# Optimization experiments

Measured on AMD Instinct MI355X. Metric: run time of the kernel, lower is better.

## Reference

```python
import jax, jax.numpy as jnp
import numpy as np
from jax import lax

KSIZE = 3
STRIDE = 1
RATE = 2
FUSE_K = 3
SCALE = 10.0
DN = ('NCHW', 'OIHW', 'NCHW')


def _same_pad_amount(size, k, s):
    out = (size + s - 1) // s
    pad = max(0, (out - 1) * s + k - size)
    return pad // 2, pad - pad // 2


def extract_patches(x, k, s):
    # torch.nn.Unfold with 'same' padding; returns [B, L, C, k, k], L row-major
    B, C, H, W = x.shape
    pt, pb = _same_pad_amount(H, k, s)
    pl, pr = _same_pad_amount(W, k, s)
    xp = jnp.pad(x, ((0, 0), (0, 0), (pt, pb), (pl, pr)))
    Ho = (H + s - 1) // s
    Wo = (W + s - 1) // s
    rows = (jnp.arange(Ho) * s)[:, None] + jnp.arange(k)[None, :]  # [Ho,k]
    cols = (jnp.arange(Wo) * s)[:, None] + jnp.arange(k)[None, :]  # [Wo,k]
    p = xp[:, :, rows, :][:, :, :, :, cols]  # [B,C,Ho,k,Wo,k]
    return p.transpose(0, 2, 4, 1, 3, 5).reshape(B, Ho * Wo, C, k, k)


def setup_inputs() -> dict:
    key = jax.random.key(0)
    kf, kb = jax.random.split(key)
    f = jax.random.normal(kf, (2, 128, 128, 128), dtype=jnp.float32)
    b = jax.random.normal(kb, (2, 128, 128, 128), dtype=jnp.float32)
    mask = jnp.zeros((1, 1, 128, 128), dtype=jnp.float32)  # all patches available
    return {"f": f, "b": b, "mask": mask}


def reference(f, b, mask):
    B, C, Hr, Wr = f.shape
    kernel = 2 * RATE
    # raw background patches for final aggregation: [B, Lb, C, 4, 4]
    raw_w = extract_patches(b, kernel, RATE * STRIDE)
    # nearest downsample by rate (src_idx = i*rate)
    f_ds = f[:, :, ::RATE, ::RATE]
    b_ds = b[:, :, ::RATE, ::RATE]
    Hf, Wf = f_ds.shape[2], f_ds.shape[3]
    Hb, Wb = b_ds.shape[2], b_ds.shape[3]
    L = Hb * Wb
    # matching patches: [B, L, C, 3, 3]
    w = extract_patches(b_ds, KSIZE, STRIDE)
    # mask patches (shared across batch, torch uses m[0])
    m_ds = mask[:, :, ::RATE, ::RATE]
    m = extract_patches(m_ds, KSIZE, STRIDE)[0]  # [L,1,3,3]
    mm = (jnp.mean(m, axis=(1, 2, 3)) == 0.0).astype(f.dtype).reshape(1, L, 1, 1)
    # L2-normalize patch filters (escape_NaN added elementwise before sum, as in torch)
    wn = w / jnp.sqrt(jnp.sum(w * w + 1e-4, axis=(2, 3, 4), keepdims=True))

    def score_one(xi, wi):
        # xi [C,Hf,Wf], wi [L,C,3,3] -> [L,Hf,Wf]
        return lax.conv_general_dilated(xi[None], wi, (1, 1), [(1, 1), (1, 1)],
                                        dimension_numbers=DN)[0]

    y = jax.vmap(score_one)(f_ds, wn)  # [B, L, Hf, Wf]

    # diagonal fuse: identity 3x3 conv on the [L, Hf*Wf] score matrix, twice with transpose
    fw = jnp.eye(FUSE_K, dtype=f.dtype).reshape(1, 1, FUSE_K, FUSE_K)

    def fuse_conv(t):
        return lax.conv_general_dilated(t, fw, (1, 1), [(1, 1), (1, 1)],
                                        dimension_numbers=DN)

    y = y.reshape(B, 1, Hb * Wb, Hf * Wf)
    y = fuse_conv(y).reshape(B, Hb, Wb, Hf, Wf)
    y = y.transpose(0, 2, 1, 4, 3).reshape(B, 1, L, Hf * Wf)
    y = fuse_conv(y).reshape(B, Wb, Hb, Wf, Hf)
    y = y.transpose(0, 2, 1, 4, 3).reshape(B, L, Hf, Wf)

    y = y * mm
    y = jax.nn.softmax(y * SCALE, axis=1) * mm

    def deconv_one(a, wc):
        # conv_transpose2d(a, wc, stride=rate, padding=1); wc [L,C,4,4]
        wt = jnp.flip(wc, (-2, -1)).transpose(1, 0, 2, 3)  # [C,L,4,4]
        pad = kernel - 1 - 1
        return lax.conv_general_dilated(a[None], wt, (1, 1), [(pad, pad), (pad, pad)],
                                        lhs_dilation=(RATE, RATE),
                                        dimension_numbers=DN)[0]

    out = jax.vmap(deconv_one)(y, raw_w) / 4.0  # [B, C, Hr, Wr]
    return out
```

## Files before the change

### kernel.cpp

```cpp
#include <hip/hip_runtime.h>
#include <cstdint>

typedef _Float16 f16x8 __attribute__((ext_vector_type(8)));
typedef float f32x4 __attribute__((ext_vector_type(4)));

typedef __attribute__((address_space(1))) void gvoid;
typedef __attribute__((address_space(3))) void lvoid;

__device__ __forceinline__ void gload16(const void* g, void* l) {
    __builtin_amdgcn_global_load_lds((gvoid*)g, (lvoid*)l, 16, 0, 0);
}

__device__ __forceinline__ void bar() {
    asm volatile("" ::: "memory");
    __builtin_amdgcn_s_barrier();
    asm volatile("" ::: "memory");
}
#define WAITV(N) asm volatile("s_waitcnt vmcnt(" #N ")" ::: "memory")
#define WAITL(N) do { asm volatile("s_waitcnt lgkmcnt(" #N ")" ::: "memory"); \
                      __builtin_amdgcn_sched_barrier(0); } while (0)

__global__ __launch_bounds__(256) void downsample_kernel(const float* __restrict__ f,
                                                         const float* __restrict__ b,
                                                         float* __restrict__ fds,
                                                         float* __restrict__ bds) {
    int idx = blockIdx.x * 256 + threadIdx.x;
    const float* src = blockIdx.y ? b : f;
    float* dst = blockIdx.y ? bds : fds;
    int bb = idx >> 19;
    int r = idx & 524287;
    int c = r >> 12, a = (r >> 6) & 63, v = r & 63;
    dst[idx] = src[(size_t)bb * 2097152 + (size_t)c * 16384 + (2 * a) * 128 + 2 * v];
}

__global__ __launch_bounds__(256) void build_mm_kernel(const float* __restrict__ mask,
                                                       float* __restrict__ mm) {
    int l = blockIdx.x * 256 + threadIdx.x;
    if (l >= 4096) return;
    int i = l >> 6, j = l & 63;
    float s = 0.f;
    #pragma unroll
    for (int dy = 0; dy < 3; ++dy)
        #pragma unroll
        for (int dx = 0; dx < 3; ++dx) {
            int a = i + dy - 1, b = j + dx - 1;
            if ((unsigned)a < 64u && (unsigned)b < 64u)
                s += mask[(2 * a) * 128 + 2 * b];
        }
    mm[l] = (s == 0.0f) ? 1.0f : 0.0f;
}

__global__ __launch_bounds__(256) void build_fpatch_kernel(const float* __restrict__ fds,
                                                           _Float16* __restrict__ Fp) {
    int bb = blockIdx.x >> 12;
    int p = blockIdx.x & 4095;
    const float* fb = fds + (size_t)bb * 524288;
    _Float16* Fpb = Fp + (size_t)bb * 4718592;
    int u = p >> 6, v = p & 63;
    for (int k = threadIdx.x; k < 1152; k += 256) {
        int c = k / 9;
        int s = k - 9 * c;
        int dy = s / 3, dx = s - 3 * dy;
        int a = u + dy - 1, bcol = v + dx - 1;
        float val = 0.f;
        if ((unsigned)a < 64u && (unsigned)bcol < 64u)
            val = fb[c * 4096 + a * 64 + bcol];
        Fpb[(size_t)p * 1152 + k] = (_Float16)val;
    }
}

__global__ __launch_bounds__(256) void build_wn_kernel(const float* __restrict__ bds,
                                                       _Float16* __restrict__ Wn) {
    __shared__ float wsh[1152];
    __shared__ float red[4];
    int bb = blockIdx.x >> 12;
    int l = blockIdx.x & 4095;
    const float* bp = bds + (size_t)bb * 524288;
    _Float16* Wnb = Wn + (size_t)bb * 4718592;
    int i = l >> 6, j = l & 63;
    float sq = 0.f;
    for (int k = threadIdx.x; k < 1152; k += 256) {
        int c = k / 9;
        int s = k - 9 * c;
        int dy = s / 3, dx = s - 3 * dy;
        int a = i + dy - 1, bcol = j + dx - 1;
        float val = 0.f;
        if ((unsigned)a < 64u && (unsigned)bcol < 64u)
            val = bp[c * 4096 + a * 64 + bcol];
        wsh[k] = val;
        sq += val * val;
    }
    #pragma unroll
    for (int off = 32; off > 0; off >>= 1) sq += __shfl_xor(sq, off);
    if ((threadIdx.x & 63) == 0) red[threadIdx.x >> 6] = sq;
    __syncthreads();
    float total = red[0] + red[1] + red[2] + red[3] + 0.1152f;
    float rinv = 1.0f / sqrtf(total);
    for (int k = threadIdx.x; k < 1152; k += 256)
        Wnb[(size_t)l * 1152 + k] = (_Float16)(wsh[k] * rinv);
}

__global__ __launch_bounds__(256) void build_vt_kernel(const float* __restrict__ b,
                                                       _Float16* __restrict__ Vt) {
    int bb = blockIdx.x >> 11;
    int n = blockIdx.x & 2047;
    const float* bp = b + (size_t)bb * 2097152;
    _Float16* Vtb = Vt + (size_t)bb * 8388608;
    int c = n >> 4, r = n & 15, rh = r >> 2, rw = r & 3;
    const float* bc = bp + (size_t)c * 16384;
    for (int l = threadIdx.x; l < 4096; l += 256) {
        int lh = l >> 6, lw = l & 63;
        int row = 2 * lh + rh - 1, col = 2 * lw + rw - 1;
        float val = 0.f;
        if ((unsigned)row < 128u && (unsigned)col < 128u)
            val = bc[row * 128 + col];
        Vtb[(size_t)n * 4096 + l] = (_Float16)val;
    }
}

template <int KSTR, int NTILES>
__device__ __forceinline__ void gemm_core(const _Float16* __restrict__ A,
                                          const _Float16* __restrict__ Bt,
                                          _Float16* __restrict__ C,
                                          _Float16* __restrict__ AsB,
                                          _Float16* __restrict__ BsB) {
    const int tid = threadIdx.x;
    const int lane = tid & 63;
    const int wave = tid >> 6;
    const int quad = lane >> 4;
    const int l16 = lane & 15;
    const int wm = wave >> 2;
    const int wn = wave & 3;
    const int bm = blockIdx.y * 256;
    const int bn = blockIdx.x * 256;

    f32x4 acc[8][4] = {};
    f16x8 afrA[4], afrB[4], bfrA[4], bfrB[4];

    const int s0 = tid, s1 = 512 + tid;
    const int sr0 = s0 >> 2, sr1 = s1 >> 2;
    const int r0 = sr0 ^ ((sr0 >> 2) & 1);
    const int r1 = sr1 ^ ((sr1 >> 2) & 1);
    const int q0 = (s0 & 3) ^ (r0 & 3);
    const int q1 = (s1 & 3) ^ (r1 & 3);
    const int offA0 = (bm + r0) * KSTR + q0 * 8;
    const int offA1 = (bm + r1) * KSTR + q1 * 8;
    const int offB0 = (bn + r0) * KSTR + q0 * 8;
    const int offB1 = (bn + r1) * KSTR + q1 * 8;

#define STAGE_A(buf, kt, kh) do {                                                          \
        gload16(A + offA0 + (kt) * 64 + (kh) * 32, AsB + ((buf) * 2 + (kh)) * 8192 + tid * 8); \
        gload16(A + offA1 + (kt) * 64 + (kh) * 32, AsB + ((buf) * 2 + (kh)) * 8192 + 4096 + tid * 8); \
    } while (0)
#define STAGE_B(buf, kt, kh) do {                                                          \
        gload16(Bt + offB0 + (kt) * 64 + (kh) * 32, BsB + ((buf) * 2 + (kh)) * 8192 + tid * 8); \
        gload16(Bt + offB1 + (kt) * 64 + (kh) * 32, BsB + ((buf) * 2 + (kh)) * 8192 + 4096 + tid * 8); \
    } while (0)

    const int c2 = (l16 >> 2) & 1;
    const int rdoff = ((l16 ^ c2) * 32) + ((quad ^ (l16 & 3)) * 8);

#define LDA(dst, buf, kh, mh) do {                                                         \
        _Pragma("unroll")                                                                  \
        for (int mi = 0; mi < 4; ++mi)                                                     \
            dst[mi] = *(const f16x8*)&AsB[((buf) * 2 + (kh)) * 8192 +                      \
                (wm * 128 + ((mh) * 4 + mi) * 16) * 32 + rdoff];                           \
    } while (0)
#define LDB(dst, buf, kh) do {                                                             \
        _Pragma("unroll")                                                                  \
        for (int ni = 0; ni < 4; ++ni)                                                     \
            dst[ni] = *(const f16x8*)&BsB[((buf) * 2 + (kh)) * 8192 +                      \
                (wn * 64 + ni * 16) * 32 + rdoff];                                         \
    } while (0)
#define MM(af, bf, mh) do {                                                                \
        __builtin_amdgcn_s_setprio(1);                                                     \
        _Pragma("unroll")                                                                  \
        for (int mi = 0; mi < 4; ++mi)                                                     \
            _Pragma("unroll")                                                              \
            for (int ni = 0; ni < 4; ++ni)                                                 \
                acc[(mh) * 4 + mi][ni] = __builtin_amdgcn_mfma_f32_16x16x32_f16(           \
                    af[mi], bf[ni], acc[(mh) * 4 + mi][ni], 0, 0, 0);                      \
        __builtin_amdgcn_s_setprio(0);                                                     \
    } while (0)

    STAGE_A(0, 0, 0); STAGE_B(0, 0, 0);
    STAGE_A(0, 0, 1); STAGE_B(0, 0, 1);
    STAGE_A(1, 1, 0); STAGE_B(1, 1, 0);
    WAITV(4);
    bar();
    LDA(afrA, 0, 0, 0); LDB(bfrA, 0, 0);

    #pragma unroll 1
    for (int i = 0; i < NTILES / 2 - 1; ++i) {
        const int t0 = 2 * i;
        STAGE_A(1, t0 + 1, 1);
        bar();
        LDA(afrB, 0, 0, 1);
        WAITL(4);
        MM(afrA, bfrA, 0);
        bar();
        STAGE_B(1, t0 + 1, 1);
        bar();
        LDA(afrA, 0, 1, 0); LDB(bfrB, 0, 1);
        WAITL(8);
        MM(afrB, bfrA, 1);
        bar();
        STAGE_A(0, t0 + 2, 0);
        bar();
        LDA(afrB, 0, 1, 1);
        WAITL(4);
        MM(afrA, bfrB, 0);
        bar();
        STAGE_B(0, t0 + 2, 0); WAITV(4);
        bar();
        LDA(afrA, 1, 0, 0); LDB(bfrA, 1, 0);
        WAITL(8);
        MM(afrB, bfrB, 1);
        bar();
        STAGE_A(0, t0 + 2, 1);
        bar();
        LDA(afrB, 1, 0, 1);
        WAITL(4);
        MM(afrA, bfrA, 0);
        bar();
        STAGE_B(0, t0 + 2, 1);
        bar();
        LDA(afrA, 1, 1, 0); LDB(bfrB, 1, 1);
        WAITL(8);
        MM(afrB, bfrA, 1);
        bar();
        STAGE_A(1, t0 + 3, 0);
        bar();
        LDA(afrB, 1, 1, 1);
        WAITL(4);
        MM(afrA, bfrB, 0);
        bar();
        STAGE_B(1, t0 + 3, 0); WAITV(4);
        bar();
        LDA(afrA, 0, 0, 0); LDB(bfrA, 0, 0);
        WAITL(8);
        MM(afrB, bfrB, 1);
        bar();
    }

    STAGE_A(1, NTILES - 1, 1);
    bar();
    LDA(afrB, 0, 0, 1);
    WAITL(4);
    MM(afrA, bfrA, 0);
    bar();
    STAGE_B(1, NTILES - 1, 1);
    bar();
    LDA(afrA, 0, 1, 0); LDB(bfrB, 0, 1);
    WAITL(8);
    MM(afrB, bfrA, 1);
    bar();
    bar();
    LDA(afrB, 0, 1, 1);
    WAITL(4);
    MM(afrA, bfrB, 0);
    bar();
    WAITV(4);
    bar();
    LDA(afrA, 1, 0, 0); LDB(bfrA, 1, 0);
    WAITL(8);
    MM(afrB, bfrB, 1);
    bar();
    bar();
    LDA(afrB, 1, 0, 1);
    WAITL(4);
    MM(afrA, bfrA, 0);
    bar();
    WAITV(0);
    bar();
    LDA(afrA, 1, 1, 0); LDB(bfrB, 1, 1);
    WAITL(8);
    MM(afrB, bfrA, 1);
    bar();
    bar();
    LDA(afrB, 1, 1, 1);
    WAITL(4);
    MM(afrA, bfrB, 0);
    bar();
    WAITL(0);
    MM(afrB, bfrB, 1);

#undef STAGE_A
#undef STAGE_B
#undef LDA
#undef LDB
#undef MM

    #pragma unroll
    for (int mi = 0; mi < 8; ++mi)
        #pragma unroll
        for (int ni = 0; ni < 4; ++ni)
            #pragma unroll
            for (int r = 0; r < 4; ++r) {
                int row = bm + wm * 128 + mi * 16 + quad * 4 + r;
                int col = bn + wn * 64 + ni * 16 + l16;
                C[(size_t)row * 4096 + col] = (_Float16)acc[mi][ni][r];
            }
}

__global__ __launch_bounds__(512, 2) void gemm1_kernel(const _Float16* __restrict__ Fp,
                                                       const _Float16* __restrict__ Wn,
                                                       _Float16* __restrict__ S0) {
    __shared__ __align__(16) _Float16 As[2][2][8192];
    __shared__ __align__(16) _Float16 Bs[2][2][8192];
    const int z = blockIdx.z;
    gemm_core<1152, 18>(Fp + (size_t)z * 4718592, Wn + (size_t)z * 4718592,
                        S0 + (size_t)z * 16777216, &As[0][0][0], &Bs[0][0][0]);
}

__global__ __launch_bounds__(512, 2) void gemm2_kernel(const _Float16* __restrict__ Vt,
                                                       const _Float16* __restrict__ att0,
                                                       const _Float16* __restrict__ att1,
                                                       _Float16* __restrict__ OTh) {
    __shared__ __align__(16) _Float16 As[2][2][8192];
    __shared__ __align__(16) _Float16 Bs[2][2][8192];
    const int z = blockIdx.z;
    gemm_core<4096, 64>(Vt + (size_t)z * 8388608, z ? att1 : att0,
                        OTh + (size_t)z * 8388608, &As[0][0][0], &Bs[0][0][0]);
}

__global__ __launch_bounds__(256) void fuse_softmax_kernel(const _Float16* __restrict__ S0,
                                                           const float* __restrict__ mm,
                                                           _Float16* __restrict__ att0,
                                                           _Float16* __restrict__ att1) {
    __shared__ float red[4];
    const int tid = threadIdx.x;
    const int lane = tid & 63;
    const int wave = tid >> 6;
    int g = blockIdx.x;
    int p_global = ((g & 7) << 10) | (g >> 3);
    const int bb = p_global >> 12;
    const int p = p_global & 4095;
    const _Float16* S = S0 + (size_t)bb * 16777216;
    _Float16* att = bb ? att1 : att0;
    const int pbase = ((p & 63) << 6) | (p >> 6);

    float acc[16];
    #pragma unroll
    for (int k = 0; k < 16; ++k) acc[k] = 0.f;

    #pragma unroll
    for (int t2 = -1; t2 <= 1; ++t2) {
        int b2 = pbase + t2;
        if ((unsigned)b2 >= 4096u) continue;
        int pp = ((b2 & 63) << 6) | (b2 >> 6);
        #pragma unroll
        for (int t1 = -1; t1 <= 1; ++t1) {
            int rr = pp + t1;
            if ((unsigned)rr >= 4096u) continue;
            const _Float16* row = S + (size_t)rr * 4096;
            #pragma unroll
            for (int k = 0; k < 16; ++k) {
                int l = k * 256 + tid;
                int i = (k * 256 + wave * 64) >> 6;
                int it2 = i + t2;
                if (it2 >= 0 && it2 < 64) {
                    int c = l + t2 * 64 + t1;
                    if ((unsigned)c < 4096u)
                        acc[k] += (float)row[c];
                } else if (it2 == 64) {
                    if (lane <= 62) {
                        int c = lane + 1 + t1;
                        if ((unsigned)c < 4096u) acc[k] += (float)row[c];
                    }
                } else {
                    if (lane >= 1) {
                        int c = 4031 + lane + t1;
                        if ((unsigned)c < 4096u) acc[k] += (float)row[c];
                    }
                }
            }
        }
    }

    float mv[16];
    float lmax = -1e30f;
    #pragma unroll
    for (int k = 0; k < 16; ++k) {
        int l = k * 256 + tid;
        mv[k] = mm[l];
        float lg = acc[k] * mv[k] * 10.0f;
        acc[k] = lg;
        lmax = fmaxf(lmax, lg);
    }
    #pragma unroll
    for (int off = 32; off > 0; off >>= 1) lmax = fmaxf(lmax, __shfl_xor(lmax, off));
    if (lane == 0) red[wave] = lmax;
    __syncthreads();
    lmax = fmaxf(fmaxf(red[0], red[1]), fmaxf(red[2], red[3]));
    __syncthreads();

    float lsum = 0.f;
    #pragma unroll
    for (int k = 0; k < 16; ++k) {
        float e = __expf(acc[k] - lmax);
        acc[k] = e;
        lsum += e;
    }
    #pragma unroll
    for (int off = 32; off > 0; off >>= 1) lsum += __shfl_xor(lsum, off);
    if (lane == 0) red[wave] = lsum;
    __syncthreads();
    float inv = 1.0f / (red[0] + red[1] + red[2] + red[3]);
    #pragma unroll
    for (int k = 0; k < 16; ++k) {
        int l = k * 256 + tid;
        att[(size_t)p * 4096 + l] = (_Float16)(acc[k] * inv * mv[k]);
    }
}

__global__ __launch_bounds__(256) void assemble_kernel(const _Float16* __restrict__ OTh,
                                                       float* __restrict__ out) {
    int idx = blockIdx.x * 256 + threadIdx.x;
    int bb = idx >> 21;
    int w = idx & 2097151;
    const _Float16* OTb = OTh + (size_t)bb * 8388608;
    int x = w & 127, y = (w >> 7) & 127, c = w >> 14;
    int r0 = (y + 1) & 1, s0 = (x + 1) & 1;
    float acc = 0.f;
    #pragma unroll
    for (int a = 0; a < 2; ++a) {
        int rh = r0 + 2 * a;
        int ph = (y + 1 - rh) >> 1;
        if ((unsigned)ph < 64u) {
            #pragma unroll
            for (int bq = 0; bq < 2; ++bq) {
                int rw = s0 + 2 * bq;
                int pw = (x + 1 - rw) >> 1;
                if ((unsigned)pw < 64u)
                    acc += (float)OTb[(size_t)(c * 16 + rh * 4 + rw) * 4096 + ph * 64 + pw];
            }
        }
    }
    out[idx] = 0.25f * acc;
}

extern "C" void kernel_launch(void* const* d_in, const int* in_sizes, int n_in,
                              void* d_out, int out_size, void* d_ws, size_t ws_size,
                              hipStream_t stream) {
    const float* f = (const float*)d_in[0];
    const float* b = (const float*)d_in[1];
    const float* mask = (const float*)d_in[2];
    float* out = (float*)d_out;
    char* ws = (char*)d_ws;

    float* mm = (float*)ws;
    _Float16* Fp = (_Float16*)(ws + 16384);
    _Float16* Wn = (_Float16*)(ws + 16384 + 18874368);
    _Float16* att0 = (_Float16*)(ws + 16384);
    _Float16* S0 = (_Float16*)(ws + 37765120);
    _Float16* Vt = (_Float16*)(ws + 37765120);
    _Float16* OTh = (_Float16*)(ws + 37765120 + 33554432);
    float* fds = (float*)(ws + 104873984);
    float* bds = (float*)(ws + 104873984 + 4194304);
    _Float16* att1 = (_Float16*)(ws + 104873984);

    downsample_kernel<<<dim3(4096, 2), 256, 0, stream>>>(f, b, fds, bds);
    build_mm_kernel<<<16, 256, 0, stream>>>(mask, mm);
    build_fpatch_kernel<<<8192, 256, 0, stream>>>(fds, Fp);
    build_wn_kernel<<<8192, 256, 0, stream>>>(bds, Wn);

    gemm1_kernel<<<dim3(16, 16, 2), 512, 0, stream>>>(Fp, Wn, S0);
    fuse_softmax_kernel<<<8192, 256, 0, stream>>>(S0, mm, att0, att1);

    build_vt_kernel<<<4096, 256, 0, stream>>>(b, Vt);
    gemm2_kernel<<<dim3(16, 8, 2), 512, 0, stream>>>(Vt, att0, att1, OTh);
    assemble_kernel<<<16384, 256, 0, stream>>>(OTh, out);
}
```

Measured before the change: 440.3 us.

## Use 4-wave 128x128 warp tiles in GEMMs and vectorize fuse-softmax row access

The shared GEMM core drops from 8 waves to 4 waves per 256x256 block. Each wave now owns a 128x128 sub-tile with 8x8 accumulators, and each thread issues four async global-to-LDS loads per stage instead of two, with the wait counts adjusted to match. The fuse-softmax kernel changes so each thread handles 16 contiguous columns: it loads the neighbouring window with two 8-wide f16 vector loads and stores the results as vectors, replacing 16 strided scalar accesses. The aim is more MFMA work per LDS fragment load and fewer memory instructions. The cost is much higher register pressure and fewer waves to hide latency, with launch bounds set to 256 threads and 1 block.

New measurement: 470.7 us. 6.9% more time.

```diff
diff --git a/kernel.cpp b/kernel.cpp
--- a/kernel.cpp
+++ b/kernel.cpp
@@ -129,32 +129,36 @@
     const int wave = tid >> 6;
     const int quad = lane >> 4;
     const int l16 = lane & 15;
-    const int wm = wave >> 2;
-    const int wn = wave & 3;
+    const int wm = wave >> 1;
+    const int wn2 = wave & 1;
     const int bm = blockIdx.y * 256;
     const int bn = blockIdx.x * 256;
 
-    f32x4 acc[8][4] = {};
-    f16x8 afrA[4], afrB[4], bfrA[4], bfrB[4];
-
-    const int s0 = tid, s1 = 512 + tid;
-    const int sr0 = s0 >> 2, sr1 = s1 >> 2;
-    const int r0 = sr0 ^ ((sr0 >> 2) & 1);
-    const int r1 = sr1 ^ ((sr1 >> 2) & 1);
-    const int q0 = (s0 & 3) ^ (r0 & 3);
-    const int q1 = (s1 & 3) ^ (r1 & 3);
-    const int offA0 = (bm + r0) * KSTR + q0 * 8;
-    const int offA1 = (bm + r1) * KSTR + q1 * 8;
-    const int offB0 = (bn + r0) * KSTR + q0 * 8;
-    const int offB1 = (bn + r1) * KSTR + q1 * 8;
+    f32x4 acc[8][8] = {};
+    f16x8 afrA[4], afrB[4], bfrA[8], bfrB[8];
+
+    int offA[4], offB[4];
+    #pragma unroll
+    for (int rd = 0; rd < 4; ++rd) {
+        int s = rd * 256 + tid;
+        int sr = s >> 2;
+        int r = sr ^ ((sr >> 2) & 1);
+        int q = (s & 3) ^ (r & 3);
+        offA[rd] = (bm + r) * KSTR + q * 8;
+        offB[rd] = (bn + r) * KSTR + q * 8;
+    }
 
 #define STAGE_A(buf, kt, kh) do {                                                          \
-        gload16(A + offA0 + (kt) * 64 + (kh) * 32, AsB + ((buf) * 2 + (kh)) * 8192 + tid * 8); \
-        gload16(A + offA1 + (kt) * 64 + (kh) * 32, AsB + ((buf) * 2 + (kh)) * 8192 + 4096 + tid * 8); \
+        _Pragma("unroll")                                                                  \
+        for (int rd = 0; rd < 4; ++rd)                                                     \
+            gload16(A + offA[rd] + (kt) * 64 + (kh) * 32,                                  \
+                    AsB + ((buf) * 2 + (kh)) * 8192 + (rd * 256 + tid) * 8);               \
     } while (0)
 #define STAGE_B(buf, kt, kh) do {                                                          \
-        gload16(Bt + offB0 + (kt) * 64 + (kh) * 32, BsB + ((buf) * 2 + (kh)) * 8192 + tid * 8); \
-        gload16(Bt + offB1 + (kt) * 64 + (kh) * 32, BsB + ((buf) * 2 + (kh)) * 8192 + 4096 + tid * 8); \
+        _Pragma("unroll")                                                                  \
+        for (int rd = 0; rd < 4; ++rd)                                                     \
+            gload16(Bt + offB[rd] + (kt) * 64 + (kh) * 32,                                 \
+                    BsB + ((buf) * 2 + (kh)) * 8192 + (rd * 256 + tid) * 8);               \
     } while (0)
 
     const int c2 = (l16 >> 2) & 1;
@@ -168,16 +172,16 @@
     } while (0)
 #define LDB(dst, buf, kh) do {                                                             \
         _Pragma("unroll")                                                                  \
-        for (int ni = 0; ni < 4; ++ni)                                                     \
+        for (int ni = 0; ni < 8; ++ni)                                                     \
             dst[ni] = *(const f16x8*)&BsB[((buf) * 2 + (kh)) * 8192 +                      \
-                (wn * 64 + ni * 16) * 32 + rdoff];                                         \
+                (wn2 * 128 + ni * 16) * 32 + rdoff];                                       \
     } while (0)
 #define MM(af, bf, mh) do {                                                                \
         __builtin_amdgcn_s_setprio(1);                                                     \
         _Pragma("unroll")                                                                  \
         for (int mi = 0; mi < 4; ++mi)                                                     \
             _Pragma("unroll")                                                              \
-            for (int ni = 0; ni < 4; ++ni)                                                 \
+            for (int ni = 0; ni < 8; ++ni)                                                 \
                 acc[(mh) * 4 + mi][ni] = __builtin_amdgcn_mfma_f32_16x16x32_f16(           \
                     af[mi], bf[ni], acc[(mh) * 4 + mi][ni], 0, 0, 0);                      \
         __builtin_amdgcn_s_setprio(0);                                                     \
@@ -186,7 +190,7 @@
     STAGE_A(0, 0, 0); STAGE_B(0, 0, 0);
     STAGE_A(0, 0, 1); STAGE_B(0, 0, 1);
     STAGE_A(1, 1, 0); STAGE_B(1, 1, 0);
-    WAITV(4);
+    WAITV(8);
     bar();
     LDA(afrA, 0, 0, 0); LDB(bfrA, 0, 0);
 
@@ -202,7 +206,7 @@
         STAGE_B(1, t0 + 1, 1);
         bar();
         LDA(afrA, 0, 1, 0); LDB(bfrB, 0, 1);
-        WAITL(8);
+        WAITL(12);
         MM(afrB, bfrA, 1);
         bar();
         STAGE_A(0, t0 + 2, 0);
@@ -211,10 +215,10 @@
         WAITL(4);
         MM(afrA, bfrB, 0);
         bar();
-        STAGE_B(0, t0 + 2, 0); WAITV(4);
+        STAGE_B(0, t0 + 2, 0); WAITV(8);
         bar();
         LDA(afrA, 1, 0, 0); LDB(bfrA, 1, 0);
-        WAITL(8);
+        WAITL(12);
         MM(afrB, bfrB, 1);
         bar();
         STAGE_A(0, t0 + 2, 1);
@@ -226,7 +230,7 @@
         STAGE_B(0, t0 + 2, 1);
         bar();
         LDA(afrA, 1, 1, 0); LDB(bfrB, 1, 1);
-        WAITL(8);
+        WAITL(12);
         MM(afrB, bfrA, 1);
         bar();
         STAGE_A(1, t0 + 3, 0);
@@ -235,10 +239,10 @@
         WAITL(4);
         MM(afrA, bfrB, 0);
         bar();
-        STAGE_B(1, t0 + 3, 0); WAITV(4);
+        STAGE_B(1, t0 + 3, 0); WAITV(8);
         bar();
         LDA(afrA, 0, 0, 0); LDB(bfrA, 0, 0);
-        WAITL(8);
+        WAITL(12);
         MM(afrB, bfrB, 1);
         bar();
     }
@@ -252,7 +256,7 @@
     STAGE_B(1, NTILES - 1, 1);
     bar();
     LDA(afrA, 0, 1, 0); LDB(bfrB, 0, 1);
-    WAITL(8);
+    WAITL(12);
     MM(afrB, bfrA, 1);
     bar();
     bar();
@@ -260,10 +264,10 @@
     WAITL(4);
     MM(afrA, bfrB, 0);
     bar();
-    WAITV(4);
+    WAITV(8);
     bar();
     LDA(afrA, 1, 0, 0); LDB(bfrA, 1, 0);
-    WAITL(8);
+    WAITL(12);
     MM(afrB, bfrB, 1);
     bar();
     bar();
@@ -274,7 +278,7 @@
     WAITV(0);
     bar();
     LDA(afrA, 1, 1, 0); LDB(bfrB, 1, 1);
-    WAITL(8);
+    WAITL(12);
     MM(afrB, bfrA, 1);
     bar();
     bar();
@@ -294,16 +298,16 @@
     #pragma unroll
     for (int mi = 0; mi < 8; ++mi)
         #pragma unroll
-        for (int ni = 0; ni < 4; ++ni)
+        for (int ni = 0; ni < 8; ++ni)
             #pragma unroll
             for (int r = 0; r < 4; ++r) {
                 int row = bm + wm * 128 + mi * 16 + quad * 4 + r;
-                int col = bn + wn * 64 + ni * 16 + l16;
+                int col = bn + wn2 * 128 + ni * 16 + l16;
                 C[(size_t)row * 4096 + col] = (_Float16)acc[mi][ni][r];
             }
 }
 
-__global__ __launch_bounds__(512, 2) void gemm1_kernel(const _Float16* __restrict__ Fp,
+__global__ __launch_bounds__(256, 1) void gemm1_kernel(const _Float16* __restrict__ Fp,
                                                        const _Float16* __restrict__ Wn,
                                                        _Float16* __restrict__ S0) {
     __shared__ __align__(16) _Float16 As[2][2][8192];
@@ -313,7 +317,7 @@
                         S0 + (size_t)z * 16777216, &As[0][0][0], &Bs[0][0][0]);
 }
 
-__global__ __launch_bounds__(512, 2) void gemm2_kernel(const _Float16* __restrict__ Vt,
+__global__ __launch_bounds__(256, 1) void gemm2_kernel(const _Float16* __restrict__ Vt,
                                                        const _Float16* __restrict__ att0,
                                                        const _Float16* __restrict__ att1,
                                                        _Float16* __restrict__ OTh) {
@@ -340,40 +344,47 @@
     _Float16* att = bb ? att1 : att0;
     const int pbase = ((p & 63) << 6) | (p >> 6);
 
+    const int i  = tid >> 2;
+    const int j0 = (tid & 3) << 4;
+    const int l0 = tid * 16;
+
     float acc[16];
     #pragma unroll
-    for (int k = 0; k < 16; ++k) acc[k] = 0.f;
+    for (int e = 0; e < 16; ++e) acc[e] = 0.f;
 
     #pragma unroll
     for (int t2 = -1; t2 <= 1; ++t2) {
         int b2 = pbase + t2;
         if ((unsigned)b2 >= 4096u) continue;
         int pp = ((b2 & 63) << 6) | (b2 >> 6);
+        const int it2 = i + t2;
         #pragma unroll
         for (int t1 = -1; t1 <= 1; ++t1) {
             int rr = pp + t1;
             if ((unsigned)rr >= 4096u) continue;
             const _Float16* row = S + (size_t)rr * 4096;
-            #pragma unroll
-            for (int k = 0; k < 16; ++k) {
-                int l = k * 256 + tid;
-                int i = (k * 256 + wave * 64) >> 6;
-                int it2 = i + t2;
-                if (it2 >= 0 && it2 < 64) {
-                    int c = l + t2 * 64 + t1;
-                    if ((unsigned)c < 4096u)
-                        acc[k] += (float)row[c];
-                } else if (it2 == 64) {
-                    if (lane <= 62) {
-                        int c = lane + 1 + t1;
-                        if ((unsigned)c < 4096u) acc[k] += (float)row[c];
-                    }
-                } else {
-                    if (lane >= 1) {
-                        int c = 4031 + lane + t1;
-                        if ((unsigned)c < 4096u) acc[k] += (float)row[c];
-                    }
+            if ((unsigned)it2 < 64u) {
+                const int ws = it2 * 64 + j0 - 1;
+                float w[18];
+                f16x8 v0 = *(const f16x8*)&row[ws + 1];
+                f16x8 v1 = *(const f16x8*)&row[ws + 9];
+                w[0]  = (ws >= 0) ? (float)row[ws] : 0.f;
+                #pragma unroll
+                for (int x = 0; x < 8; ++x) {
+                    w[1 + x] = (float)v0[x];
+                    w[9 + x] = (float)v1[x];
                 }
+                w[17] = (ws + 17 < 4096) ? (float)row[ws + 17] : 0.f;
+                #pragma unroll
+                for (int e = 0; e < 16; ++e) acc[e] += w[e + 1 + t1];
+            } else if (it2 == 64) {
+                #pragma unroll
+                for (int e = 0; e < 16; ++e)
+                    if (j0 + e <= 62) acc[e] += (float)row[j0 + e + 1 + t1];
+            } else {
+                #pragma unroll
+                for (int e = 0; e < 16; ++e)
+                    if (j0 + e >= 1) acc[e] += (float)row[4031 + j0 + e + t1];
             }
         }
     }
@@ -381,11 +392,10 @@
     float mv[16];
     float lmax = -1e30f;
     #pragma unroll
-    for (int k = 0; k < 16; ++k) {
-        int l = k * 256 + tid;
-        mv[k] = mm[l];
-        float lg = acc[k] * mv[k] * 10.0f;
-        acc[k] = lg;
+    for (int e = 0; e < 16; ++e) {
+        mv[e] = mm[l0 + e];
+        float lg = acc[e] * mv[e] * 10.0f;
+        acc[e] = lg;
         lmax = fmaxf(lmax, lg);
     }
     #pragma unroll
@@ -397,21 +407,23 @@
 
     float lsum = 0.f;
     #pragma unroll
-    for (int k = 0; k < 16; ++k) {
-        float e = __expf(acc[k] - lmax);
-        acc[k] = e;
-        lsum += e;
+    for (int e = 0; e < 16; ++e) {
+        float ex = __expf(acc[e] - lmax);
+        acc[e] = ex;
+        lsum += ex;
     }
     #pragma unroll
     for (int off = 32; off > 0; off >>= 1) lsum += __shfl_xor(lsum, off);
     if (lane == 0) red[wave] = lsum;
     __syncthreads();
     float inv = 1.0f / (red[0] + red[1] + red[2] + red[3]);
-    #pragma unroll
-    for (int k = 0; k < 16; ++k) {
-        int l = k * 256 + tid;
-        att[(size_t)p * 4096 + l] = (_Float16)(acc[k] * inv * mv[k]);
-    }
+
+    _Float16 outv[16];
+    #pragma unroll
+    for (int e = 0; e < 16; ++e) outv[e] = (_Float16)(acc[e] * inv * mv[e]);
+    _Float16* dst = att + (size_t)p * 4096 + l0;
+    *(f16x8*)&dst[0] = *(const f16x8*)&outv[0];
+    *(f16x8*)&dst[8] = *(const f16x8*)&outv[8];
 }
 
 __global__ __launch_bounds__(256) void assemble_kernel(const _Float16* __restrict__ OTh,
@@ -465,10 +477,10 @@
     build_fpatch_kernel<<<8192, 256, 0, stream>>>(fds, Fp);
     build_wn_kernel<<<8192, 256, 0, stream>>>(bds, Wn);
 
-    gemm1_kernel<<<dim3(16, 16, 2), 512, 0, stream>>>(Fp, Wn, S0);
+    gemm1_kernel<<<dim3(16, 16, 2), 256, 0, stream>>>(Fp, Wn, S0);
     fuse_softmax_kernel<<<8192, 256, 0, stream>>>(S0, mm, att0, att1);
 
     build_vt_kernel<<<4096, 256, 0, stream>>>(b, Vt);
-    gemm2_kernel<<<dim3(16, 8, 2), 512, 0, stream>>>(Vt, att0, att1, OTh);
+    gemm2_kernel<<<dim3(16, 8, 2), 256, 0, stream>>>(Vt, att0, att1, OTh);
     assemble_kernel<<<16384, 256, 0, stream>>>(OTh, out);
 }
```
